# Performance work log

Measured on AMD Instinct MI355X. Metric: run time of the kernel, lower is better.

The kernel has to match this reference:

```python
import jax, jax.numpy as jnp
import numpy as np

N_NODES = 100000
N_EDGES = 1600000
N_GRAPHS = 256
DIMS = [128, 128, 128, 128]  # gcn_layers_dim -> 3 GCNConv layers


def setup_inputs() -> dict:
    key = jax.random.key(0)
    ks = jax.random.split(key, 12)
    inp = {
        "x": jax.random.normal(ks[0], (N_NODES, DIMS[0]), jnp.float32),
        "edge_index": jax.random.randint(ks[1], (2, N_EDGES), 0, N_NODES),
        "edge_weight": jax.random.uniform(ks[2], (N_EDGES,), jnp.float32),
        "batch": jnp.sort(jax.random.randint(ks[3], (N_NODES,), 0, N_GRAPHS)),
    }
    for i in range(3):
        fan_in = DIMS[i]
        scale = 1.0 / np.sqrt(fan_in)
        inp[f"W{i+1}"] = jax.random.uniform(ks[4 + 2 * i], (DIMS[i], DIMS[i + 1]),
                                             jnp.float32, -scale, scale)
        inp[f"b{i+1}"] = jax.random.uniform(ks[5 + 2 * i], (DIMS[i + 1],),
                                             jnp.float32, -scale, scale)
    return inp


def reference(x, edge_index, edge_weight, batch, W1, b1, W2, b2, W3, b3):
    n = x.shape[0]
    # PyG GCNConv: add self-loops with weight 1, symmetric normalization.
    loop = jnp.arange(n)
    row = jnp.concatenate([edge_index[0], loop])  # source nodes
    col = jnp.concatenate([edge_index[1], loop])  # target nodes (aggregation index)
    w = jnp.concatenate([edge_weight, jnp.ones((n,), x.dtype)])
    deg = jax.ops.segment_sum(w, col, num_segments=n)
    dinv = jnp.where(deg > 0, jax.lax.rsqrt(deg), jnp.zeros_like(deg))
    norm = dinv[row] * w * dinv[col]  # [E+N]

    # global_mean_pool setup
    counts = jax.ops.segment_sum(jnp.ones((n,), x.dtype), batch,
                                 num_segments=N_GRAPHS)
    counts = jnp.maximum(counts, 1.0)[:, None]

    def gcn_conv(h, W, b):
        hl = h @ W                      # linear projection first (PyG order)
        msg = hl[row] * norm[:, None]   # gather + edge scaling
        out = jax.ops.segment_sum(msg, col, num_segments=n)  # scatter-add
        return out + b

    embeddings = []
    h = x
    for W, b in ((W1, b1), (W2, b2), (W3, b3)):
        h = gcn_conv(h, W, b)
        h = jax.nn.relu(h)              # relu_layers_index = [0,1,2]
        emb = jax.ops.segment_sum(h, batch, num_segments=N_GRAPHS) / counts
        embeddings.append(emb)          # gep = global_mean_pool
    return tuple(embeddings)
```

## Files before the change

### kernel.cpp

```cpp
#include <hip/hip_runtime.h>


typedef short short8 __attribute__((ext_vector_type(8)));
typedef float f32x4  __attribute__((ext_vector_type(4)));

__device__ inline unsigned pack_bf16x2(float a, float b) {
    unsigned ua = __float_as_uint(a);
    ua = (ua + 0x7FFFu + ((ua >> 16) & 1u)) >> 16;
    unsigned ub = __float_as_uint(b);
    ub = (ub + 0x7FFFu + ((ub >> 16) & 1u)) >> 16;
    return ua | (ub << 16);
}
__device__ inline ushort bf16_1(float a) {
    unsigned ua = __float_as_uint(a);
    return (ushort)((ua + 0x7FFFu + ((ua >> 16) & 1u)) >> 16);
}
__device__ inline float bf_lo(unsigned u) { return __uint_as_float(u << 16); }
__device__ inline float bf_hi(unsigned u) { return __uint_as_float(u & 0xFFFF0000u); }


template <bool F32IN>
__device__ __forceinline__ void gemm_tile(const void* __restrict__ Hin,
                                          const ushort* __restrict__ WbT,
                                          unsigned* __restrict__ O, int M,
                                          int bid, unsigned* sOut) {
    int lane = threadIdx.x & 63;
    int wv = threadIdx.x >> 6;
    int quad = lane >> 4;
    int mrow = lane & 15;
    int m0 = bid * 128 + wv * 32;
    int r0 = m0 + mrow;
    int r1 = r0 + 16;
    int r0c = r0 < M ? r0 : M - 1;
    int r1c = r1 < M ? r1 : M - 1;

    short8 a0[4], a1[4];
    if (F32IN) {
        const float* Hf = (const float*)Hin;
#pragma unroll
        for (int s = 0; s < 4; s++) {
            const float4* p0 = (const float4*)(Hf + (size_t)r0c * 128 + s * 32 + quad * 8);
            const float4* p1 = (const float4*)(Hf + (size_t)r1c * 128 + s * 32 + quad * 8);
            float4 f0 = p0[0], f1 = p0[1];
            float4 g0 = p1[0], g1 = p1[1];
            union { short8 s8; unsigned u[4]; } t0, t1;
            t0.u[0] = pack_bf16x2(f0.x, f0.y); t0.u[1] = pack_bf16x2(f0.z, f0.w);
            t0.u[2] = pack_bf16x2(f1.x, f1.y); t0.u[3] = pack_bf16x2(f1.z, f1.w);
            t1.u[0] = pack_bf16x2(g0.x, g0.y); t1.u[1] = pack_bf16x2(g0.z, g0.w);
            t1.u[2] = pack_bf16x2(g1.x, g1.y); t1.u[3] = pack_bf16x2(g1.z, g1.w);
            a0[s] = t0.s8; a1[s] = t1.s8;
        }
    } else {
        const unsigned* Hb = (const unsigned*)Hin;
#pragma unroll
        for (int s = 0; s < 4; s++) {
            a0[s] = *(const short8*)(Hb + (size_t)r0c * 64 + s * 16 + quad * 4);
            a1[s] = *(const short8*)(Hb + (size_t)r1c * 64 + s * 16 + quad * 4);
        }
    }
    f32x4 acc0[8], acc1[8];
#pragma unroll
    for (int t = 0; t < 8; t++) {
        acc0[t] = (f32x4){0.f, 0.f, 0.f, 0.f};
        acc1[t] = (f32x4){0.f, 0.f, 0.f, 0.f};
    }
#pragma unroll
    for (int s = 0; s < 4; s++) {
#pragma unroll
        for (int t = 0; t < 8; t++) {
            short8 b = *(const short8*)(WbT + (t * 16 + mrow) * 128 + s * 32 + quad * 8);
            acc0[t] = __builtin_amdgcn_mfma_f32_16x16x32_bf16(a0[s], b, acc0[t], 0, 0, 0);
            acc1[t] = __builtin_amdgcn_mfma_f32_16x16x32_bf16(a1[s], b, acc1[t], 0, 0, 0);
        }
    }
    ushort* so = (ushort*)(sOut + wv * 32 * 64);
#pragma unroll
    for (int t = 0; t < 8; t++) {
#pragma unroll
        for (int r = 0; r < 4; r++) {
            int lr = quad * 4 + r;
            int c = t * 16 + mrow;
            so[lr * 128 + c] = bf16_1(acc0[t][r]);
            so[(lr + 16) * 128 + c] = bf16_1(acc1[t][r]);
        }
    }
    __syncthreads();
    const unsigned* si = sOut + wv * 32 * 64;
#pragma unroll 8
    for (int r = 0; r < 32; r++) {
        int row = m0 + r;
        if (row < M) O[(size_t)row * 64 + lane] = si[r * 64 + lane];
    }
}

__device__ __forceinline__ void pool_tile(const unsigned* __restrict__ HB,
                                          const int* __restrict__ gb,
                                          float* __restrict__ outp, int g,
                                          float* part) {
    int lane = threadIdx.x & 63, w = threadIdx.x >> 6;
    int s = gb[g], e = gb[g + 1];
    float ax = 0.f, ay = 0.f;
    for (int i = s + w; i < e; i += 4) {
        unsigned u = HB[(size_t)i * 64 + lane];
        ax += bf_lo(u); ay += bf_hi(u);
    }
    part[w * 128 + lane * 2] = ax;
    part[w * 128 + lane * 2 + 1] = ay;
    __syncthreads();
    if (threadIdx.x < 128) {
        float sum = part[threadIdx.x] + part[128 + threadIdx.x]
                  + part[256 + threadIdx.x] + part[384 + threadIdx.x];
        float c = (float)(e - s);
        outp[g * 128 + threadIdx.x] = sum / fmaxf(c, 1.0f);
    }
}


__global__ void k_prep(const int* __restrict__ batch, int* __restrict__ gb,
                       int G, int N,
                       const float* __restrict__ W0, const float* __restrict__ W1,
                       const float* __restrict__ W2, ushort* __restrict__ WbT) {
    int id = blockIdx.x * blockDim.x + threadIdx.x;
    if (id <= G) {
        int lo = 0, hi = N;
        while (lo < hi) { int mid = (lo + hi) >> 1; if (batch[mid] < id) lo = mid + 1; else hi = mid; }
        gb[id] = lo;
    }
    if (id < 3 * 16384) {
        int l = id >> 14;
        const float* W = (l == 0) ? W0 : ((l == 1) ? W1 : W2);
        int id2 = id & 16383;
        int n = id2 & 127, k = id2 >> 7;
        WbT[l * 16384 + n * 128 + k] = bf16_1(W[k * 128 + n]);
    }
}

__global__ __launch_bounds__(256) void k_phase1(const int* __restrict__ ei,
                                                int* __restrict__ hist, int E,
                                                const float* __restrict__ x,
                                                const ushort* __restrict__ WbT,
                                                unsigned* __restrict__ O, int M,
                                                int nbGemm, int nbCount) {
    __shared__ unsigned sBuf[8192];
    if (blockIdx.x < nbGemm) {
        gemm_tile<true>(x, WbT, O, M, blockIdx.x, sBuf);
        return;
    }
    int blk = blockIdx.x - nbGemm;
    unsigned* hcnt = sBuf;
    int t = threadIdx.x;
    for (int i = t; i < nbGemm; i += 256) hcnt[i] = 0;
    __syncthreads();
    int base = blk * 8192;
    for (int i = t; i < 8192; i += 256) {
        int e = base + i;
        if (e < E) atomicAdd(&hcnt[(unsigned)ei[E + e] >> 7], 1u);
    }
    __syncthreads();
    for (int b = t; b < nbGemm; b += 256)
        hist[b * nbCount + blk] = (int)hcnt[b];
}

__global__ __launch_bounds__(1024) void k_scan1(const int* __restrict__ cnt,
                                                int* __restrict__ pre,
                                                int* __restrict__ bsum, int n) {
    __shared__ int wsum[16];
    int t = threadIdx.x, lane = t & 63, w = t >> 6;
    int i = blockIdx.x * 1024 + t;
    int v = (i < n) ? cnt[i] : 0;
    int x = v;
#pragma unroll
    for (int off = 1; off < 64; off <<= 1) {
        int y = __shfl_up(x, off, 64);
        if (lane >= off) x += y;
    }
    if (lane == 63) wsum[w] = x;
    __syncthreads();
    int woff = 0, tot = 0;
#pragma unroll
    for (int q = 0; q < 16; q++) { int s = wsum[q]; if (q < w) woff += s; tot += s; }
    if (i < n) pre[i] = woff + x - v;
    if (t == 0) bsum[blockIdx.x] = tot;
}

__global__ __launch_bounds__(256) void k_scat(const int* __restrict__ ei,
                                              const float* __restrict__ ew,
                                              const int* __restrict__ pre,
                                              const int* __restrict__ bsumRaw,
                                              int* __restrict__ bucketStart,
                                              int2* __restrict__ recs,
                                              int E, int nbkt, int nbCount,
                                              int nbScan) {
    __shared__ int sRaw[256];
    __shared__ int sPre[256];
    __shared__ int sWt[4];
    __shared__ int sBase[784];
    __shared__ unsigned rk[784];
    int t = threadIdx.x;
    sRaw[t] = (t < nbScan) ? bsumRaw[t] : 0;
    for (int b = t; b < nbkt; b += 256) rk[b] = 0;
    __syncthreads();
    int lane = t & 63, w2 = t >> 6;
    int v = sRaw[t];
    int x = v;
#pragma unroll
    for (int off = 1; off < 64; off <<= 1) {
        int y = __shfl_up(x, off, 64);
        if (lane >= off) x += y;
    }
    if (lane == 63) sWt[w2] = x;
    __syncthreads();
    int base = 0;
#pragma unroll
    for (int q = 0; q < 4; q++) { if (q < w2) base += sWt[q]; }
    sPre[t] = base + x - v;
    __syncthreads();
    int blk = blockIdx.x;
    for (int b = t; b < nbkt; b += 256) {
        int f = b * nbCount + blk;
        sBase[b] = pre[f] + sPre[f >> 10];
    }
    if (blk == 0) {
        for (int b = t; b <= nbkt; b += 256) {
            if (b == nbkt) bucketStart[b] = E;
            else { int f = b * nbCount; bucketStart[b] = pre[f] + sPre[f >> 10]; }
        }
    }
    __syncthreads();
    int e0 = blk * 8192;
    for (int i = t; i < 8192; i += 256) {
        int e = e0 + i;
        if (e < E) {
            int r = ei[e];
            int c = ei[E + e];
            float w = ew[e];
            int b = (unsigned)c >> 7;
            unsigned rank = atomicAdd(&rk[b], 1u);
            int2 rec; rec.x = r | ((c & 127) << 17); rec.y = __float_as_int(w);
            recs[sBase[b] + (int)rank] = rec;
        }
    }
}

__global__ __launch_bounds__(256) void k_fin(const int2* __restrict__ recs,
                                             const int* __restrict__ bucketStart,
                                             int2* __restrict__ csr,
                                             int* __restrict__ ptrv,
                                             float* __restrict__ dinv,
                                             int N, int nbkt) {
    __shared__ unsigned scnt[128];
    __shared__ float swdeg[128];
    __shared__ float sdinv[128];
    __shared__ unsigned sTot0;
    int t = threadIdx.x;
    int b = blockIdx.x;
    int e0 = bucketStart[b], e1 = bucketStart[b + 1];
    if (t < 128) { scnt[t] = 0u; swdeg[t] = 0.f; }
    __syncthreads();
    for (int i = e0 + t; i < e1; i += 256) {
        int2 rec = recs[i];
        int cl = (rec.x >> 17) & 127;
        atomicAdd(&scnt[cl], 1u);
        atomicAdd(&swdeg[cl], __int_as_float(rec.y));
    }
    __syncthreads();
    unsigned myc = (t < 128) ? scnt[t] : 0u;
    int lane = t & 63, wv = t >> 6;
    unsigned inc = myc;
#pragma unroll
    for (int off = 1; off < 64; off <<= 1) {
        unsigned y = __shfl_up(inc, off, 64);
        if (lane >= off) inc += y;
    }
    if (t == 63) sTot0 = inc;
    __syncthreads();
    unsigned excl = inc - myc + ((wv == 1) ? sTot0 : 0u);
    if (t < 128) {
        scnt[t] = excl;
        float dv = rsqrtf(1.0f + swdeg[t]);
        sdinv[t] = dv;
        int node = b * 128 + t;
        if (node < N) { ptrv[node] = e0 + (int)excl; dinv[node] = dv; }
    }
    if (b == nbkt - 1 && t == 0) ptrv[N] = e1;
    __syncthreads();
    for (int i = e0 + t; i < e1; i += 256) {
        int2 rec = recs[i];
        int cl = (rec.x >> 17) & 127;
        int r = rec.x & 131071;
        unsigned rank = atomicAdd(&scnt[cl], 1u);
        float y = __int_as_float(rec.y) * sdinv[cl];
        int2 mv; mv.x = r; mv.y = __float_as_int(y);
        csr[e0 + (int)rank] = mv;
    }
}

__global__ __launch_bounds__(256) void k_norm2(int2* __restrict__ csr,
                                               const float* __restrict__ dinv,
                                               int E) {
    int base = blockIdx.x * 1024 + threadIdx.x;
#pragma unroll
    for (int q = 0; q < 4; q++) {
        int e = base + q * 256;
        if (e < E) {
            int2 m = csr[e];
            m.y = __float_as_int(__int_as_float(m.y) * dinv[m.x]);
            csr[e] = m;
        }
    }
}

__global__ __launch_bounds__(256) void k_agg(const unsigned* __restrict__ HL,
                                             const int* __restrict__ ptr,
                                             const int2* __restrict__ csr,
                                             const float* __restrict__ dinv,
                                             const float* __restrict__ bias,
                                             unsigned* __restrict__ Hout, int M) {
    __shared__ int2 sM[4 * 64];
    int node = (int)((blockIdx.x * blockDim.x + threadIdx.x) >> 6);
    if (node >= M) return;
    int lane = threadIdx.x & 63;
    int half = lane >> 5;
    int q = lane & 31;
    int2* mbase = &sM[(threadIdx.x >> 6) * 64];
    int e0 = ptr[node], e1 = ptr[node + 1];
    int deg = e1 - e0;
    int nbv = deg < 64 ? deg : 64;
    if (lane < nbv) mbase[lane] = csr[e0 + lane];
    const uint2* HL2 = (const uint2*)HL;
    float di = dinv[node];
    float sn = (half == 0) ? di * di : 0.f;
    uint2 us = HL2[(size_t)node * 32 + q];
    float a0 = sn * bf_lo(us.x), a1 = sn * bf_hi(us.x);
    float a2 = sn * bf_lo(us.y), a3 = sn * bf_hi(us.y);
    int j = half;
    for (; j + 8 <= nbv; j += 8) {
        int2 m[4]; uint2 u[4];
#pragma unroll
        for (int t = 0; t < 4; t++) m[t] = mbase[j + 2 * t];
#pragma unroll
        for (int t = 0; t < 4; t++) u[t] = HL2[(size_t)m[t].x * 32 + q];
#pragma unroll
        for (int t = 0; t < 4; t++) {
            float nv = __int_as_float(m[t].y);
            a0 += nv * bf_lo(u[t].x); a1 += nv * bf_hi(u[t].x);
            a2 += nv * bf_lo(u[t].y); a3 += nv * bf_hi(u[t].y);
        }
    }
    for (; j < nbv; j += 2) {
        int2 m = mbase[j];
        uint2 u = HL2[(size_t)m.x * 32 + q];
        float nv = __int_as_float(m.y);
        a0 += nv * bf_lo(u.x); a1 += nv * bf_hi(u.x);
        a2 += nv * bf_lo(u.y); a3 += nv * bf_hi(u.y);
    }
    for (int e = e0 + 64 + half; e < e1; e += 2) {
        int2 m = csr[e];
        uint2 u = HL2[(size_t)m.x * 32 + q];
        float nv = __int_as_float(m.y);
        a0 += nv * bf_lo(u.x); a1 += nv * bf_hi(u.x);
        a2 += nv * bf_lo(u.y); a3 += nv * bf_hi(u.y);
    }
    a0 += __shfl_xor(a0, 32, 64);
    a1 += __shfl_xor(a1, 32, 64);
    a2 += __shfl_xor(a2, 32, 64);
    a3 += __shfl_xor(a3, 32, 64);
    float4 bv = ((const float4*)bias)[q];
    float r0 = fmaxf(a0 + bv.x, 0.f);
    float r1 = fmaxf(a1 + bv.y, 0.f);
    float r2 = fmaxf(a2 + bv.z, 0.f);
    float r3 = fmaxf(a3 + bv.w, 0.f);
    if (half == 0) {
        uint2 pv;
        pv.x = pack_bf16x2(r0, r1);
        pv.y = pack_bf16x2(r2, r3);
        ((uint2*)(Hout + (size_t)node * 64))[q] = pv;
    }
}

__global__ __launch_bounds__(256) void k_gemm_pool(const unsigned* __restrict__ Hb,
                                                   const ushort* __restrict__ WbT,
                                                   unsigned* __restrict__ O, int M,
                                                   const int* __restrict__ gb,
                                                   float* __restrict__ outp,
                                                   int nbGemm) {
    __shared__ unsigned sBuf[8192];
    if (blockIdx.x < nbGemm) {
        gemm_tile<false>(Hb, WbT, O, M, blockIdx.x, sBuf);
        return;
    }
    pool_tile(Hb, gb, outp, blockIdx.x - nbGemm, (float*)sBuf);
}

extern "C" void kernel_launch(void* const* d_in, const int* in_sizes, int n_in,
                              void* d_out, int out_size, void* d_ws, size_t ws_size,
                              hipStream_t stream) {
    const float* x     = (const float*)d_in[0];
    const int*   ei    = (const int*)d_in[1];
    const float* ew    = (const float*)d_in[2];
    const int*   batch = (const int*)d_in[3];
    const float* Wt[3] = {(const float*)d_in[4], (const float*)d_in[6], (const float*)d_in[8]};
    const float* bt[3] = {(const float*)d_in[5], (const float*)d_in[7], (const float*)d_in[9]};
    float* out = (float*)d_out;

    const int D = 128;
    const int N = in_sizes[0] / D;
    const int E = in_sizes[2];
    const int G = out_size / (3 * D);

    char* p = (char*)d_ws;
    auto alloc = [&](size_t bytes) {
        void* r = (void*)p;
        p += (bytes + 255) & ~(size_t)255;
        return r;
    };
    int nbkt    = (N + 127) / 128;
    int nbCount = (E + 8191) / 8192;
    int F       = nbkt * nbCount;
    int nbScan  = (F + 1023) / 1024;

    int*      ptr    = (int*)alloc((size_t)(N + 1) * 4);
    int*      bsum   = (int*)alloc((size_t)256 * 4);
    int*      gb     = (int*)alloc((size_t)(G + 1) * 4);
    int*      bstart = (int*)alloc((size_t)(nbkt + 1) * 4);
    float*    dinv   = (float*)alloc((size_t)N * 4);
    ushort*   WbT    = (ushort*)alloc((size_t)3 * 16384 * 2);
    int2*     csr    = (int2*)alloc((size_t)E * 8);
    unsigned* bufHL  = (unsigned*)alloc((size_t)N * 64 * 4);
    unsigned* bufH   = (unsigned*)alloc((size_t)N * 64 * 4);
    int*  hist = (int*)csr;
    int*  pre  = hist + F;
    int2* recs = (int2*)bufH;

    int nbGemm = (N + 127) / 128;
    int prepWork = 3 * 16384;

    k_prep<<<(prepWork + 255) / 256, 256, 0, stream>>>(batch, gb, G, N,
                                                       Wt[0], Wt[1], Wt[2], WbT);
    k_phase1<<<nbGemm + nbCount, 256, 0, stream>>>(ei, hist, E, x, WbT,
                                                   bufHL, N, nbGemm, nbCount);
    k_scan1<<<nbScan, 1024, 0, stream>>>(hist, pre, bsum, F);
    k_scat<<<nbCount, 256, 0, stream>>>(ei, ew, pre, bsum, bstart, recs,
                                        E, nbkt, nbCount, nbScan);
    k_fin<<<nbkt, 256, 0, stream>>>(recs, bstart, csr, ptr, dinv, N, nbkt);
    k_norm2<<<(E + 1023) / 1024, 256, 0, stream>>>(csr, dinv, E);

    k_agg<<<(N + 3) / 4, 256, 0, stream>>>(bufHL, ptr, csr, dinv, bt[0], bufH, N);
    k_gemm_pool<<<nbGemm + G, 256, 0, stream>>>(bufH, WbT + 16384, bufHL, N,
                                                gb, out + 0 * (size_t)G * D, nbGemm);
    k_agg<<<(N + 3) / 4, 256, 0, stream>>>(bufHL, ptr, csr, dinv, bt[1], bufH, N);
    k_gemm_pool<<<nbGemm + G, 256, 0, stream>>>(bufH, WbT + 2 * 16384, bufHL, N,
                                                gb, out + 1 * (size_t)G * D, nbGemm);
    k_agg<<<(N + 3) / 4, 256, 0, stream>>>(bufHL, ptr, csr, dinv, bt[2], bufH, N);
    k_gemm_pool<<<G, 256, 0, stream>>>(bufH, WbT, nullptr, 0,
                                       gb, out + 2 * (size_t)G * D, 0);
}
```

Measured before the change: 524.5 us.

## Fold self-loops into CSR as explicit edges and deepen gather unroll in aggregation

The CSR build now reserves one slot per node for its self-loop: each node's segment starts with an entry (node, dinv), which the normalization pass scales by dinv again. Aggregation can then drop the separate dinv load and self-term handling. The aggregation loop also gains an 8-way unrolled gather stage that keeps more neighbor loads in flight. In exchange, the CSR array and normalization pass grow by N entries, the self-loop now counts toward the 64-entry staged neighbor cap, and register pressure rises from the wider unroll.

```diff
diff --git a/kernel.cpp b/kernel.cpp
--- a/kernel.cpp
+++ b/kernel.cpp
@@ -255,6 +255,7 @@
     int t = threadIdx.x;
     int b = blockIdx.x;
     int e0 = bucketStart[b], e1 = bucketStart[b + 1];
+    int FB = e0 + b * 128;
     if (t < 128) { scnt[t] = 0u; swdeg[t] = 0.f; }
     __syncthreads();
     for (int i = e0 + t; i < e1; i += 256) {
@@ -276,13 +277,19 @@
     __syncthreads();
     unsigned excl = inc - myc + ((wv == 1) ? sTot0 : 0u);
     if (t < 128) {
-        scnt[t] = excl;
         float dv = rsqrtf(1.0f + swdeg[t]);
         sdinv[t] = dv;
+        scnt[t] = excl + (unsigned)t + 1u;
         int node = b * 128 + t;
-        if (node < N) { ptrv[node] = e0 + (int)excl; dinv[node] = dv; }
-    }
-    if (b == nbkt - 1 && t == 0) ptrv[N] = e1;
+        int start = FB + (int)excl + t;
+        if (node < N) {
+            ptrv[node] = start;
+            dinv[node] = dv;
+            int2 sv; sv.x = node; sv.y = __float_as_int(dv);
+            csr[start] = sv;
+        }
+    }
+    if (b == nbkt - 1 && t == 0) ptrv[N] = e1 + N;
     __syncthreads();
     for (int i = e0 + t; i < e1; i += 256) {
         int2 rec = recs[i];
@@ -291,7 +298,7 @@
         unsigned rank = atomicAdd(&scnt[cl], 1u);
         float y = __int_as_float(rec.y) * sdinv[cl];
         int2 mv; mv.x = r; mv.y = __float_as_int(y);
-        csr[e0 + (int)rank] = mv;
+        csr[FB + (int)rank] = mv;
     }
 }
 
@@ -313,7 +320,6 @@
 __global__ __launch_bounds__(256) void k_agg(const unsigned* __restrict__ HL,
                                              const int* __restrict__ ptr,
                                              const int2* __restrict__ csr,
-                                             const float* __restrict__ dinv,
                                              const float* __restrict__ bias,
                                              unsigned* __restrict__ Hout, int M) {
     __shared__ int2 sM[4 * 64];
@@ -328,12 +334,21 @@
     int nbv = deg < 64 ? deg : 64;
     if (lane < nbv) mbase[lane] = csr[e0 + lane];
     const uint2* HL2 = (const uint2*)HL;
-    float di = dinv[node];
-    float sn = (half == 0) ? di * di : 0.f;
-    uint2 us = HL2[(size_t)node * 32 + q];
-    float a0 = sn * bf_lo(us.x), a1 = sn * bf_hi(us.x);
-    float a2 = sn * bf_lo(us.y), a3 = sn * bf_hi(us.y);
+    float a0 = 0.f, a1 = 0.f, a2 = 0.f, a3 = 0.f;
     int j = half;
+    for (; j + 16 <= nbv; j += 16) {
+        int2 m[8]; uint2 u[8];
+#pragma unroll
+        for (int t = 0; t < 8; t++) m[t] = mbase[j + 2 * t];
+#pragma unroll
+        for (int t = 0; t < 8; t++) u[t] = HL2[(size_t)m[t].x * 32 + q];
+#pragma unroll
+        for (int t = 0; t < 8; t++) {
+            float nv = __int_as_float(m[t].y);
+            a0 += nv * bf_lo(u[t].x); a1 += nv * bf_hi(u[t].x);
+            a2 += nv * bf_lo(u[t].y); a3 += nv * bf_hi(u[t].y);
+        }
+    }
     for (; j + 8 <= nbv; j += 8) {
         int2 m[4]; uint2 u[4];
 #pragma unroll
@@ -425,7 +440,7 @@
     int*      bstart = (int*)alloc((size_t)(nbkt + 1) * 4);
     float*    dinv   = (float*)alloc((size_t)N * 4);
     ushort*   WbT    = (ushort*)alloc((size_t)3 * 16384 * 2);
-    int2*     csr    = (int2*)alloc((size_t)E * 8);
+    int2*     csr    = (int2*)alloc((size_t)(E + N) * 8);
     unsigned* bufHL  = (unsigned*)alloc((size_t)N * 64 * 4);
     unsigned* bufH   = (unsigned*)alloc((size_t)N * 64 * 4);
     int*  hist = (int*)csr;
@@ -443,15 +458,15 @@
     k_scat<<<nbCount, 256, 0, stream>>>(ei, ew, pre, bsum, bstart, recs,
                                         E, nbkt, nbCount, nbScan);
     k_fin<<<nbkt, 256, 0, stream>>>(recs, bstart, csr, ptr, dinv, N, nbkt);
-    k_norm2<<<(E + 1023) / 1024, 256, 0, stream>>>(csr, dinv, E);
-
-    k_agg<<<(N + 3) / 4, 256, 0, stream>>>(bufHL, ptr, csr, dinv, bt[0], bufH, N);
+    k_norm2<<<(E + N + 1023) / 1024, 256, 0, stream>>>(csr, dinv, E + N);
+
+    k_agg<<<(N + 3) / 4, 256, 0, stream>>>(bufHL, ptr, csr, bt[0], bufH, N);
     k_gemm_pool<<<nbGemm + G, 256, 0, stream>>>(bufH, WbT + 16384, bufHL, N,
                                                 gb, out + 0 * (size_t)G * D, nbGemm);
-    k_agg<<<(N + 3) / 4, 256, 0, stream>>>(bufHL, ptr, csr, dinv, bt[1], bufH, N);
+    k_agg<<<(N + 3) / 4, 256, 0, stream>>>(bufHL, ptr, csr, bt[1], bufH, N);
     k_gemm_pool<<<nbGemm + G, 256, 0, stream>>>(bufH, WbT + 2 * 16384, bufHL, N,
                                                 gb, out + 1 * (size_t)G * D, nbGemm);
-    k_agg<<<(N + 3) / 4, 256, 0, stream>>>(bufHL, ptr, csr, dinv, bt[2], bufH, N);
+    k_agg<<<(N + 3) / 4, 256, 0, stream>>>(bufHL, ptr, csr, bt[2], bufH, N);
     k_gemm_pool<<<G, 256, 0, stream>>>(bufH, WbT, nullptr, 0,
                                        gb, out + 2 * (size_t)G * D, 0);
 }
```

Result: no change. 524.4 us (-0.0%).
